# Optimization experiments

Measured on AMD Instinct MI355X. Metric: run time of the kernel, lower is better.

## Reference

```python
import jax, jax.numpy as jnp
import numpy as np

B, F, K = 1024, 512, 16


def setup_inputs() -> dict:
    key = jax.random.key(0)
    k1, k2, k3, k4 = jax.random.split(key, 4)
    x = jax.random.normal(k1, (B, F), dtype=jnp.float32)
    W = jax.random.normal(k2, (F, K), dtype=jnp.float32) * (6.0 / (F + K)) ** 0.5
    lin_w = jax.random.normal(k3, (1, F), dtype=jnp.float32) * 0.02
    lin_b = jax.random.normal(k4, (1,), dtype=jnp.float32) * 0.02
    return {"x": x, "W": W, "lin_w": lin_w, "lin_b": lin_b}


# Static lower-triangular mask (includes diagonal), flattened over F*F.
_TRIL_MASK = np.tril(np.ones((F, F), dtype=bool)).reshape(-1)


def reference(x, W, lin_w, lin_b):
    # Linear part: (B, F) @ (F, 1) + b -> (B, 1)
    p1 = x @ lin_w.T + lin_b  # (B, 1)

    # Order-2 cross term (faithful to the original, including the
    # reshape -- NOT transpose -- of WX before the bmm).
    WX = x[:, :, None] * W  # (B, F, K)
    WX_r = WX.reshape(B, K, F)  # reshape, not transpose (matches torch code)
    out = jnp.matmul(WX, WX_r)  # (B, F, F)
    out_flat = out.reshape(B, F * F)[:, _TRIL_MASK]  # (B, F*(F+1)/2)
    p2 = jnp.sum(out_flat, axis=1, keepdims=True)  # (B, 1)

    return jax.nn.sigmoid(p1 + p2)
```

## Files before the change

kernel.cpp:

```cpp
#include <hip/hip_runtime.h>
#include <math.h>

constexpr int Bn = 1024;
constexpr int Fn = 512;
constexpr int Kn = 16;
constexpr int CSTRIDE = 520;

__global__ __launch_bounds__(512) void fm_kernel(
    const float* __restrict__ x,
    const float* __restrict__ W,
    const float* __restrict__ lin_w,
    const float* __restrict__ lin_b,
    float* __restrict__ out)
{
    const int b = blockIdx.x;
    const int t = threadIdx.x;
    const int k = t >> 5;
    const int q = t & 31;

    __shared__ float WXc[Kn * CSTRIDE];
    __shared__ float red[8];

    const float xv = x[(size_t)b * Fn + t];

    const float4* Wrow = reinterpret_cast<const float4*>(W + (size_t)t * Kn);
    const float4 w0 = Wrow[0], w1 = Wrow[1], w2 = Wrow[2], w3 = Wrow[3];

    float row[16] = {xv*w0.x, xv*w0.y, xv*w0.z, xv*w0.w,
                     xv*w1.x, xv*w1.y, xv*w1.z, xv*w1.w,
                     xv*w2.x, xv*w2.y, xv*w2.z, xv*w2.w,
                     xv*w3.x, xv*w3.y, xv*w3.z, xv*w3.w};

    const int fs = t ^ (t >> 5);
    #pragma unroll
    for (int kk = 0; kk < Kn; ++kk)
        WXc[kk * CSTRIDE + fs] = row[kk];

    __syncthreads();

    float col[16];
    const int base = k * CSTRIDE;
    #pragma unroll
    for (int r = 0; r < 16; ++r) {
        const int u = (q << 4) + r;
        col[r] = WXc[base + (u ^ (u >> 5))];
    }

    float G = 0.f;
    #pragma unroll
    for (int r = 0; r < 16; ++r) G += col[r];

    float incl = G;
    #pragma unroll
    for (int d = 1; d < 32; d <<= 1) {
        const float o = __shfl_down(incl, d, 32);
        if (q + d < 32) incl += o;
    }
    const float Tq = incl - G;

    float S = 0.f, acc = 0.f;
    #pragma unroll
    for (int r = 15; r >= 0; --r) {
        S += col[r];
        acc = fmaf(row[r], Tq + S, acc);
    }

    acc = fmaf(xv, lin_w[t], acc);

    #pragma unroll
    for (int d = 32; d >= 1; d >>= 1)
        acc += __shfl_xor(acc, d);

    if ((t & 63) == 0) red[t >> 6] = acc;
    __syncthreads();
    if (t == 0) {
        float tot = red[0] + red[1] + red[2] + red[3]
                  + red[4] + red[5] + red[6] + red[7];
        tot += lin_b[0];
        out[b] = 1.0f / (1.0f + expf(-tot));
    }
}

extern "C" void kernel_launch(void* const* d_in, const int* in_sizes, int n_in,
                              void* d_out, int out_size, void* d_ws, size_t ws_size,
                              hipStream_t stream) {
    const float* x     = (const float*)d_in[0];
    const float* W     = (const float*)d_in[1];
    const float* lin_w = (const float*)d_in[2];
    const float* lin_b = (const float*)d_in[3];
    float* out = (float*)d_out;

    hipLaunchKernelGGL(fm_kernel, dim3(Bn), dim3(512), 0, stream,
                       x, W, lin_w, lin_b, out);
}
```

Measured before the change: 9.685 us.

## Factor x out of cross term, drop LDS staging, process two rows per block

```diff
diff --git a/kernel.cpp b/kernel.cpp
--- a/kernel.cpp
+++ b/kernel.cpp
@@ -4,80 +4,79 @@
 constexpr int Bn = 1024;
 constexpr int Fn = 512;
 constexpr int Kn = 16;
-constexpr int CSTRIDE = 520;
+constexpr int BPB = 2;
 
-__global__ __launch_bounds__(512) void fm_kernel(
+__global__ __launch_bounds__(512, 4) void fm_kernel(
     const float* __restrict__ x,
     const float* __restrict__ W,
     const float* __restrict__ lin_w,
     const float* __restrict__ lin_b,
     float* __restrict__ out)
 {
-    const int b = blockIdx.x;
     const int t = threadIdx.x;
     const int k = t >> 5;
     const int q = t & 31;
+    const int b0 = blockIdx.x * BPB;
 
-    __shared__ float WXc[Kn * CSTRIDE];
-    __shared__ float red[8];
+    __shared__ float red[BPB][8];
 
-    const float xv = x[(size_t)b * Fn + t];
+    const float4* Wrow4 = reinterpret_cast<const float4*>(W + t * Kn);
+    const float4 a0 = Wrow4[0], a1 = Wrow4[1], a2 = Wrow4[2], a3 = Wrow4[3];
+    const float wr[16] = {a0.x, a0.y, a0.z, a0.w, a1.x, a1.y, a1.z, a1.w,
+                          a2.x, a2.y, a2.z, a2.w, a3.x, a3.y, a3.z, a3.w};
 
-    const float4* Wrow = reinterpret_cast<const float4*>(W + (size_t)t * Kn);
-    const float4 w0 = Wrow[0], w1 = Wrow[1], w2 = Wrow[2], w3 = Wrow[3];
+    float wt[16];
+    #pragma unroll
+    for (int u = 0; u < 16; ++u)
+        wt[u] = W[(16 * q + u) * Kn + k];
 
-    float row[16] = {xv*w0.x, xv*w0.y, xv*w0.z, xv*w0.w,
-                     xv*w1.x, xv*w1.y, xv*w1.z, xv*w1.w,
-                     xv*w2.x, xv*w2.y, xv*w2.z, xv*w2.w,
-                     xv*w3.x, xv*w3.y, xv*w3.z, xv*w3.w};
+    float Wrsum = 0.f;
+    #pragma unroll
+    for (int r = 0; r < 16; ++r) Wrsum += wr[r];
 
-    const int fs = t ^ (t >> 5);
+    const float lw = lin_w[t];
+
     #pragma unroll
-    for (int kk = 0; kk < Kn; ++kk)
-        WXc[kk * CSTRIDE + fs] = row[kk];
+    for (int bb = 0; bb < BPB; ++bb) {
+        const float* xb = x + (size_t)(b0 + bb) * Fn;
+
+        const float4* xq4 = reinterpret_cast<const float4*>(xb + 16 * q);
+        const float4 c0 = xq4[0], c1 = xq4[1], c2 = xq4[2], c3 = xq4[3];
+        const float xq[16] = {c0.x, c0.y, c0.z, c0.w, c1.x, c1.y, c1.z, c1.w,
+                              c2.x, c2.y, c2.z, c2.w, c3.x, c3.y, c3.z, c3.w};
+        const float xs = xb[t];
+
+        float S = 0.f, acc2 = 0.f;
+        #pragma unroll
+        for (int r = 15; r >= 0; --r) {
+            S    = fmaf(xq[r], wt[r], S);
+            acc2 = fmaf(wr[r], S, acc2);
+        }
+        const float G = S;
+
+        float incl = G;
+        #pragma unroll
+        for (int d = 1; d < 32; d <<= 1) {
+            const float o = __shfl_down(incl, d, 32);
+            if (q + d < 32) incl += o;
+        }
+        const float Tq = incl - G;
+
+        float part = xs * (acc2 + Tq * Wrsum + lw);
+
+        #pragma unroll
+        for (int d = 32; d >= 1; d >>= 1)
+            part += __shfl_xor(part, d);
+        if ((t & 63) == 0) red[bb][t >> 6] = part;
+    }
 
     __syncthreads();
 
-    float col[16];
-    const int base = k * CSTRIDE;
-    #pragma unroll
-    for (int r = 0; r < 16; ++r) {
-        const int u = (q << 4) + r;
-        col[r] = WXc[base + (u ^ (u >> 5))];
-    }
-
-    float G = 0.f;
-    #pragma unroll
-    for (int r = 0; r < 16; ++r) G += col[r];
-
-    float incl = G;
-    #pragma unroll
-    for (int d = 1; d < 32; d <<= 1) {
-        const float o = __shfl_down(incl, d, 32);
-        if (q + d < 32) incl += o;
-    }
-    const float Tq = incl - G;
-
-    float S = 0.f, acc = 0.f;
-    #pragma unroll
-    for (int r = 15; r >= 0; --r) {
-        S += col[r];
-        acc = fmaf(row[r], Tq + S, acc);
-    }
-
-    acc = fmaf(xv, lin_w[t], acc);
-
-    #pragma unroll
-    for (int d = 32; d >= 1; d >>= 1)
-        acc += __shfl_xor(acc, d);
-
-    if ((t & 63) == 0) red[t >> 6] = acc;
-    __syncthreads();
-    if (t == 0) {
-        float tot = red[0] + red[1] + red[2] + red[3]
-                  + red[4] + red[5] + red[6] + red[7];
+    if (t < BPB) {
+        float tot = red[t][0] + red[t][1] + red[t][2] + red[t][3]
+                  + red[t][4] + red[t][5] + red[t][6] + red[t][7];
         tot += lin_b[0];
-        out[b] = 1.0f / (1.0f + expf(-tot));
+        out[b0 + t] = 1.0f / (1.0f + expf(-tot));
     }
 }
 
@@ -90,6 +89,6 @@
     const float* lin_b = (const float*)d_in[3];
     float* out = (float*)d_out;
 
-    hipLaunchKernelGGL(fm_kernel, dim3(Bn), dim3(512), 0, stream,
+    hipLaunchKernelGGL(fm_kernel, dim3(Bn / BPB), dim3(512), 0, stream,
                        x, W, lin_w, lin_b, out);
 }
```

Result: slower. 16.97 us (+75.2%).
